# Optimization experiments

Measured on AMD Instinct MI355X. Metric: run time of the kernel, lower is better.

Reference implementation:

```python
import jax, jax.numpy as jnp
import numpy as np

B, N, F, DM, DMO, OM, L = 32, 64, 64, 128, 64, 128, 4
PRE_H, PRE_O, POST_H = 128, 64, 64
E = N * N
EPS = 1e-5


def swish(x):
    return x * jax.nn.sigmoid(x)


def bn_edges(x, g, b):
    # BatchNorm1d(num_features=E) applied to [B, E, D]: per-edge-channel stats over (batch, D)
    m = x.mean(axis=(0, 2), keepdims=True)
    v = x.var(axis=(0, 2), keepdims=True)
    return (x - m) / jnp.sqrt(v + EPS) * g[None, :, None] + b[None, :, None]


def setup_inputs():
    key = jax.random.key(0)
    ks = iter(jax.random.split(key, 64))

    def rn(shape, s=0.05):
        return jax.random.normal(next(ks), shape, dtype=jnp.float32) * s

    # fully-connected graph incl. self-loops (required by BatchNorm1d(n_nodes^2))
    src, dst = np.meshgrid(np.arange(N), np.arange(N), indexing='ij')
    edge_index = jnp.asarray(np.stack([src.reshape(-1), dst.reshape(-1)]), dtype=jnp.int32)
    return {
        'node_feature': rn((B, N, F), 1.0),
        'vectors': rn((B, N, OM), 1.0),
        'edge_index': edge_index,
        'msg_W1': rn((L, 2 * F, DM)), 'msg_b1': rn((L, DM)),
        'bn1_g': jnp.ones((L, E), jnp.float32), 'bn1_b': jnp.zeros((L, E), jnp.float32),
        'msg_W2': rn((L, DM, DM)), 'msg_b2': rn((L, DM)),
        'bn2_g': jnp.ones((L, E), jnp.float32), 'bn2_b': jnp.zeros((L, E), jnp.float32),
        'msg_W3': rn((L, DM, DM)), 'msg_b3': rn((L, DM)),
        'bn3_g': jnp.ones((L, E), jnp.float32), 'bn3_b': jnp.zeros((L, E), jnp.float32),
        'msg_W4': rn((L, DM, DMO)), 'msg_b4': rn((L, DMO)),
        'upd_W1': rn((L, OM + F + DMO, DM)), 'upd_b1': rn((L, DM)),
        'upd_W2': rn((L, DM, DM)), 'upd_b2': rn((L, DM)),
        'upd_W3': rn((L, DM, DM)), 'upd_b3': rn((L, DM)),
        'upd_W4': rn((L, DM, F)), 'upd_b4': rn((L, F)),
        'pre_W1': rn((F, PRE_H)), 'pre_b1': rn((PRE_H,)),
        'pre_W2': rn((PRE_H, PRE_H)), 'pre_b2': rn((PRE_H,)),
        'pre_W3': rn((PRE_H, PRE_H)), 'pre_b3': rn((PRE_H,)),
        'pre_W4': rn((PRE_H, PRE_O)), 'pre_b4': rn((PRE_O,)),
        'post_W1': rn((PRE_O, POST_H)), 'post_b1': rn((POST_H,)),
        'post_W2': rn((POST_H, 1)), 'post_b2': rn((1,)),
    }


def reference(node_feature, vectors, edge_index,
              msg_W1, msg_b1, bn1_g, bn1_b, msg_W2, msg_b2, bn2_g, bn2_b,
              msg_W3, msg_b3, bn3_g, bn3_b, msg_W4, msg_b4,
              upd_W1, upd_b1, upd_W2, upd_b2, upd_W3, upd_b3, upd_W4, upd_b4,
              pre_W1, pre_b1, pre_W2, pre_b2, pre_W3, pre_b3, pre_W4, pre_b4,
              post_W1, post_b1, post_W2, post_b2):
    src, dst = edge_index[0], edge_index[1]
    x = node_feature  # [B, N, F]
    v = vectors       # [B, N, OM]
    cnt = jax.ops.segment_sum(jnp.ones((E,), jnp.float32), dst, num_segments=N)
    inv_cnt = 1.0 / jnp.maximum(cnt, 1.0)
    for l in range(L):
        x_i = x[:, dst]  # [B, E, F] gather targets
        x_j = x[:, src]  # [B, E, F] gather sources
        h = swish(jnp.concatenate([x_i, x_j], -1) @ msg_W1[l] + msg_b1[l])
        h = bn_edges(h, bn1_g[l], bn1_b[l])
        h = bn_edges(swish(h @ msg_W2[l] + msg_b2[l]), bn2_g[l], bn2_b[l])
        h = bn_edges(swish(h @ msg_W3[l] + msg_b3[l]), bn3_g[l], bn3_b[l])
        m = swish(h @ msg_W4[l] + msg_b4[l])  # [B, E, DMO]
        agg = jax.ops.segment_sum(jnp.transpose(m, (1, 0, 2)), dst, num_segments=N)
        agg = jnp.transpose(agg, (1, 0, 2)) * inv_cnt[None, :, None]  # mean aggr, [B, N, DMO]
        u = jnp.concatenate([v, x, agg], -1)  # [B, N, OM+F+DMO]
        h = swish(u @ upd_W1[l] + upd_b1[l])
        h = swish(h @ upd_W2[l] + upd_b2[l])
        h = swish(h @ upd_W3[l] + upd_b3[l])
        x = x + swish(h @ upd_W4[l] + upd_b4[l])  # residual update
    h = swish(x @ pre_W1 + pre_b1)
    h = swish(h @ pre_W2 + pre_b2)
    h = swish(h @ pre_W3 + pre_b3)
    h = h @ pre_W4 + pre_b4
    c = swish(h @ post_W1 + post_b1) @ post_W2 + post_b2  # [B, N, 1]
    x3 = jnp.einsum('bnd,bn->bd', v, c[..., 0])           # coefficient-weighted vector sum
    return x3, v, c
```

## Files before the change

kernel.cpp:

```cpp
#include <hip/hip_runtime.h>
#include <hip/hip_bf16.h>

typedef unsigned short u16t;
typedef __attribute__((ext_vector_type(8))) short bf16x8;
typedef __attribute__((ext_vector_type(4))) float f32x4;

#define Bn 32
#define Nn 64
#define Fd 64
#define DMd 128
#define DMOd 64
#define OMd 128
#define En 4096

#define NTEN 36
#define TOTALC 1073217
#define HP 136
#define UP 264
#define XP 72
#define WSEG 131072

__device__ const int kOffs[NTEN + 1] = {
    0,        131072,   393216,   458752,   459264,   475648,   492032,   557568,
    558080,   574464,   590848,   656384,   656896,   673280,   689664,   722432,
    722688,   853760,   854272,   919808,   920320,   985856,   986368,   1019136,
    1019392,  1027584,  1027712,  1044096,  1044224,  1060608,  1060736,  1068928,
    1068992,  1073088,  1073152,  1073216,  1073217
};

#define C_NF    0
#define C_VEC   131072
#define C_MW1   393216
#define C_MB1   458752
#define C_G1    459264
#define C_BB1   475648
#define C_MW2   492032
#define C_MB2   557568
#define C_G2    558080
#define C_BB2   574464
#define C_MW3   590848
#define C_MB3   656384
#define C_G3    656896
#define C_BB3   673280
#define C_MW4   689664
#define C_MB4   722432
#define C_UW1   722688
#define C_UB1   853760
#define C_UW2   854272
#define C_UB2   919808
#define C_UW3   920320
#define C_UB3   985856
#define C_UW4   986368
#define C_UB4   1019136
#define C_PW1   1019392
#define C_PB1   1027584
#define C_PW2   1027712
#define C_PB2   1044096
#define C_PW3   1044224
#define C_PB3   1060608
#define C_PW4   1060736
#define C_PB4   1068928
#define C_QW1   1068992
#define C_QB1   1073088
#define C_QW2   1073152
#define C_QB2   1073216

#define S_W2T 0
#define S_W3T 16384
#define S_W4T 32768
#define S_U1T 40960
#define S_U2T 73728
#define S_U3T 90112
#define S_U4T 106496
#define S_W1T 114688

struct Ptrs { const void* p[NTEN]; };

__device__ __forceinline__ float us2f(u16t u) {
    return __uint_as_float(((unsigned int)u) << 16);
}
__device__ __forceinline__ u16t f2us(float f) {
    __hip_bfloat16 h = __float2bfloat16(f);
    return *reinterpret_cast<u16t*>(&h);
}
__device__ __forceinline__ u16t f2us_fast(float f) {
    return (u16t)((__float_as_uint(f) + 0x8000u) >> 16);
}
__device__ __forceinline__ unsigned pack2(float f0, float f1) {
    return __builtin_amdgcn_perm(__float_as_uint(f1) + 0x8000u,
                                 __float_as_uint(f0) + 0x8000u, 0x07060302u);
}
__device__ __forceinline__ float swishf(float x) {
    return x * __builtin_amdgcn_rcpf(1.0f + __expf(-x));
}

__global__ void k_flag(const u16t* __restrict__ g1raw, int* __restrict__ flag) {
    if (threadIdx.x == 0) *flag = (g1raw[0] == 0x3F80u) ? 1 : 0;
}

__global__ __launch_bounds__(256) void k_convert(Ptrs t, float* __restrict__ C,
                                                 float* __restrict__ x,
                                                 const int* __restrict__ flagp) {
    int i = blockIdx.x * 256 + threadIdx.x;
    if (i >= TOTALC) return;
    const int flag = *flagp;
    int lo = 0, hi = NTEN;
    while (hi - lo > 1) { int m = (lo + hi) >> 1; if (i >= kOffs[m]) lo = m; else hi = m; }
    const int local = i - kOffs[lo];
    float v;
    if (flag) v = us2f(((const u16t*)t.p[lo])[local]);
    else      v = ((const float*)t.p[lo])[local];
    C[i] = v;
    if (i < Bn * Nn * Fd) x[i] = v;
}

__global__ __launch_bounds__(256) void k_prepw(const float* __restrict__ C,
                                               u16t* __restrict__ W) {
    int i = blockIdx.x * 256 + threadIdx.x;
    if (i >= 4 * WSEG) return;
    const int l = i / WSEG;
    int r = i - l * WSEG;
    int src;
    if (r < S_W3T)      { int q = r;          int n = q >> 7, k = q & 127; src = C_MW2 + l*16384 + k*128 + n; }
    else if (r < S_W4T) { int q = r - S_W3T;  int n = q >> 7, k = q & 127; src = C_MW3 + l*16384 + k*128 + n; }
    else if (r < S_U1T) { int q = r - S_W4T;  int n = q >> 7, k = q & 127; src = C_MW4 + l*8192  + k*64  + n; }
    else if (r < S_U2T) { int q = r - S_U1T;  int n = q >> 8, k = q & 255; src = C_UW1 + l*32768 + k*128 + n; }
    else if (r < S_U3T) { int q = r - S_U2T;  int n = q >> 7, k = q & 127; src = C_UW2 + l*16384 + k*128 + n; }
    else if (r < S_U4T) { int q = r - S_U3T;  int n = q >> 7, k = q & 127; src = C_UW3 + l*16384 + k*128 + n; }
    else if (r < S_W1T) { int q = r - S_U4T;  int n = q >> 7, k = q & 127; src = C_UW4 + l*8192  + k*64  + n; }
    else                { int q = r - S_W1T;  int n = q >> 7, k = q & 127; src = C_MW1 + l*16384 + k*128 + n; }
    W[i] = f2us(C[src]);
}

__global__ __launch_bounds__(128) void k_pq0(const float* __restrict__ x,
                                             const float* __restrict__ W1,
                                             float* __restrict__ P, float* __restrict__ Q) {
    __shared__ float xr[Fd];
    const int bn = blockIdx.x;
    const int tid = threadIdx.x;
    if (tid < Fd) xr[tid] = x[bn * Fd + tid];
    __syncthreads();
    float accP = 0.f, accQ = 0.f;
    #pragma unroll
    for (int k = 0; k < Fd; k++) {
        float xv = xr[k];
        accP += xv * W1[k * DMd + tid];
        accQ += xv * W1[(Fd + k) * DMd + tid];
    }
    P[bn * DMd + tid] = accP;
    Q[bn * DMd + tid] = accQ;
}

__device__ __forceinline__ void red8(float* s, float (*red)[8], float (*stats)[2],
                                     int wv, int lane, int tid) {
    #pragma unroll
    for (int off = 32; off > 0; off >>= 1)
        #pragma unroll
        for (int k = 0; k < 8; k++) s[k] += __shfl_down(s[k], off);
    if (lane == 0) {
        #pragma unroll
        for (int k = 0; k < 8; k++) red[wv][k] = s[k];
    }
    __syncthreads();
    if (tid < 4) {
        float S  = red[0][2*tid]   + red[1][2*tid]   + red[2][2*tid]   + red[3][2*tid];
        float S2 = red[0][2*tid+1] + red[1][2*tid+1] + red[2][2*tid+1] + red[3][2*tid+1];
        float mean = S * (1.0f / 4096.0f);
        float var  = S2 * (1.0f / 4096.0f) - mean * mean;
        stats[tid][0] = mean;
        stats[tid][1] = rsqrtf(var + 1e-5f);
    }
    __syncthreads();
}

__global__ __launch_bounds__(256, 3) void k_edge(
    const float* __restrict__ P, const float* __restrict__ Q,
    const float* __restrict__ b1v,
    const float* __restrict__ g1, const float* __restrict__ bb1,
    const u16t* __restrict__ W2t, const float* __restrict__ b2v,
    const float* __restrict__ g2, const float* __restrict__ bb2,
    const u16t* __restrict__ W3t, const float* __restrict__ b3v,
    const float* __restrict__ g3, const float* __restrict__ bb3,
    const u16t* __restrict__ W4t, const float* __restrict__ b4v,
    float* __restrict__ m_part) {
    __shared__ u16t hE[4][Bn * HP];
    __shared__ float red[4][8];
    __shared__ float stats[4][2];

    const int dst = blockIdx.x & 63, sg = blockIdx.x >> 6, src0 = sg * 4;
    const int tid = threadIdx.x;
    const int wv = tid >> 6, lane = tid & 63, quad = lane >> 4, l15 = lane & 15;
    const int mw = wv & 1, nb2 = wv >> 1;
    const int mrow = mw * 16 + l15;
    const int nBase = nb2 * 64;

    {
        const int b = tid >> 3, d0 = (tid & 7) * 16;
        float4 pv[4], bv[4];
        {
            const float4* pp = (const float4*)&P[(b * Nn + dst) * DMd + d0];
            const float4* bp = (const float4*)&b1v[d0];
            #pragma unroll
            for (int j = 0; j < 4; j++) { pv[j] = pp[j]; bv[j] = bp[j]; }
        }
        float h[4][16];
        #pragma unroll
        for (int e = 0; e < 4; e++) {
            const float4* qq = (const float4*)&Q[(b * Nn + src0 + e) * DMd + d0];
            #pragma unroll
            for (int j = 0; j < 4; j++) {
                float4 qv = qq[j];
                h[e][j*4+0] = swishf(pv[j].x + qv.x + bv[j].x);
                h[e][j*4+1] = swishf(pv[j].y + qv.y + bv[j].y);
                h[e][j*4+2] = swishf(pv[j].z + qv.z + bv[j].z);
                h[e][j*4+3] = swishf(pv[j].w + qv.w + bv[j].w);
            }
        }
        float s[8];
        #pragma unroll
        for (int e = 0; e < 4; e++) {
            float se = 0.f, s2e = 0.f;
            #pragma unroll
            for (int i = 0; i < 16; i++) { se += h[e][i]; s2e += h[e][i] * h[e][i]; }
            s[2*e] = se; s[2*e+1] = s2e;
        }
        red8(s, red, stats, wv, lane, tid);
        #pragma unroll
        for (int e = 0; e < 4; e++) {
            float a  = stats[e][1] * g1[(src0 + e) * Nn + dst];
            float cc = bb1[(src0 + e) * Nn + dst] - stats[e][0] * a;
            uint4 w0, w1;
            w0.x = pack2(h[e][0]  * a + cc, h[e][1]  * a + cc);
            w0.y = pack2(h[e][2]  * a + cc, h[e][3]  * a + cc);
            w0.z = pack2(h[e][4]  * a + cc, h[e][5]  * a + cc);
            w0.w = pack2(h[e][6]  * a + cc, h[e][7]  * a + cc);
            w1.x = pack2(h[e][8]  * a + cc, h[e][9]  * a + cc);
            w1.y = pack2(h[e][10] * a + cc, h[e][11] * a + cc);
            w1.z = pack2(h[e][12] * a + cc, h[e][13] * a + cc);
            w1.w = pack2(h[e][14] * a + cc, h[e][15] * a + cc);
            *(uint4*)&hE[e][b * HP + d0]     = w0;
            *(uint4*)&hE[e][b * HP + d0 + 8] = w1;
        }
    }
    __syncthreads();

    #pragma unroll 1
    for (int st = 0; st < 2; st++) {
        const u16t*  Wt = st ? W3t : W2t;
        const float* bv = st ? b3v : b2v;
        const float* gv = st ? g3  : g2;
        const float* bb = st ? bb3 : bb2;
        f32x4 acc[4][4];
        #pragma unroll
        for (int t = 0; t < 4; t++) {
            float b0 = bv[nBase + t * 16 + l15];
            #pragma unroll
            for (int e = 0; e < 4; e++) acc[e][t] = (f32x4){b0, b0, b0, b0};
        }
        #pragma unroll
        for (int ks = 0; ks < 4; ks++) {
            bf16x8 wb[4];
            #pragma unroll
            for (int t = 0; t < 4; t++)
                wb[t] = *(const bf16x8*)&Wt[(nBase + t * 16 + l15) * 128 + ks * 32 + quad * 8];
            #pragma unroll
            for (int e = 0; e < 4; e++) {
                bf16x8 a8 = *(const bf16x8*)&hE[e][mrow * HP + ks * 32 + quad * 8];
                #pragma unroll
                for (int t = 0; t < 4; t++)
                    acc[e][t] = __builtin_amdgcn_mfma_f32_16x16x32_bf16(a8, wb[t], acc[e][t], 0, 0, 0);
            }
        }
        float s[8];
        #pragma unroll
        for (int e = 0; e < 4; e++) {
            float se = 0.f, s2e = 0.f;
            #pragma unroll
            for (int t = 0; t < 4; t++)
                #pragma unroll
                for (int r = 0; r < 4; r++) {
                    float v = swishf(acc[e][t][r]);
                    acc[e][t][r] = v;
                    se += v; s2e += v * v;
                }
            s[2*e] = se; s[2*e+1] = s2e;
        }
        red8(s, red, stats, wv, lane, tid);
        #pragma unroll
        for (int e = 0; e < 4; e++) {
            float a  = stats[e][1] * gv[(src0 + e) * Nn + dst];
            float cc = bb[(src0 + e) * Nn + dst] - stats[e][0] * a;
            #pragma unroll
            for (int t = 0; t < 4; t++)
                #pragma unroll
                for (int r = 0; r < 4; r++)
                    hE[e][(mw * 16 + quad * 4 + r) * HP + nBase + t * 16 + l15] =
                        f2us_fast(acc[e][t][r] * a + cc);
        }
        __syncthreads();
    }

    {
        const int n40 = nb2 * 32;
        f32x4 a4[4][2];
        #pragma unroll
        for (int t = 0; t < 2; t++) {
            float b0 = b4v[n40 + t * 16 + l15];
            #pragma unroll
            for (int e = 0; e < 4; e++) a4[e][t] = (f32x4){b0, b0, b0, b0};
        }
        #pragma unroll
        for (int ks = 0; ks < 4; ks++) {
            bf16x8 wb[2];
            #pragma unroll
            for (int t = 0; t < 2; t++)
                wb[t] = *(const bf16x8*)&W4t[(n40 + t * 16 + l15) * 128 + ks * 32 + quad * 8];
            #pragma unroll
            for (int e = 0; e < 4; e++) {
                bf16x8 a8 = *(const bf16x8*)&hE[e][mrow * HP + ks * 32 + quad * 8];
                #pragma unroll
                for (int t = 0; t < 2; t++)
                    a4[e][t] = __builtin_amdgcn_mfma_f32_16x16x32_bf16(a8, wb[t], a4[e][t], 0, 0, 0);
            }
        }
        #pragma unroll
        for (int t = 0; t < 2; t++)
            #pragma unroll
            for (int r = 0; r < 4; r++) {
                float m = swishf(a4[0][t][r]) + swishf(a4[1][t][r])
                        + swishf(a4[2][t][r]) + swishf(a4[3][t][r]);
                int b = mw * 16 + quad * 4 + r;
                m_part[(size_t)sg * (Bn * Nn * DMOd) + b * (Nn * DMOd) + dst * DMOd
                       + n40 + t * 16 + l15] = m;
            }
    }
}

__global__ __launch_bounds__(256) void k_updq(
    const float* __restrict__ vC, float* __restrict__ x, const float* __restrict__ m_part,
    const u16t* __restrict__ U1t, const float* __restrict__ b1,
    const u16t* __restrict__ U2t, const float* __restrict__ b2,
    const u16t* __restrict__ U3t, const float* __restrict__ b3,
    const u16t* __restrict__ U4t, const float* __restrict__ b4,
    const u16t* __restrict__ W1Tn, float* __restrict__ Pn, float* __restrict__ Qn,
    int doPQ) {
    __shared__ u16t uL[16 * UP];
    __shared__ u16t hL[16 * HP];
    __shared__ u16t xL[16 * XP];
    __shared__ float aggL[16 * 64];
    const int bl = blockIdx.x;
    const int g0 = bl * 16;
    const int tid = threadIdx.x;
    const int wv = tid >> 6, lane = tid & 63, quad = lane >> 4, l15 = lane & 15;
    const int nBase = wv * 32;

    {
        const int bb = bl >> 2, j0 = (bl & 3) * 16;
        const int o = tid * 4;
        const float* base = m_part + (size_t)bb * (Nn * DMOd) + (j0 + (o >> 6)) * DMOd + (o & 63);
        float4 s = *(const float4*)base;
        #pragma unroll
        for (int sgi = 1; sgi < 16; sgi++) {
            float4 v = *(const float4*)(base + (size_t)sgi * (Bn * Nn * DMOd));
            s.x += v.x; s.y += v.y; s.z += v.z; s.w += v.w;
        }
        *(float4*)&aggL[o] = s;
    }
    __syncthreads();

    {
        const int i = tid >> 4, c0 = (tid & 15) * 16;
        const int g = g0 + i;
        const float* srcp; float scl = 1.f;
        if (c0 < 128)       srcp = &vC[g * OMd + c0];
        else if (c0 < 192)  srcp = &x[g * Fd + (c0 - 128)];
        else              { srcp = &aggL[i * 64 + (c0 - 192)]; scl = 1.0f / 64.0f; }
        uint4 s0, s1;
        s0.x = pack2(srcp[0]  * scl, srcp[1]  * scl);
        s0.y = pack2(srcp[2]  * scl, srcp[3]  * scl);
        s0.z = pack2(srcp[4]  * scl, srcp[5]  * scl);
        s0.w = pack2(srcp[6]  * scl, srcp[7]  * scl);
        s1.x = pack2(srcp[8]  * scl, srcp[9]  * scl);
        s1.y = pack2(srcp[10] * scl, srcp[11] * scl);
        s1.z = pack2(srcp[12] * scl, srcp[13] * scl);
        s1.w = pack2(srcp[14] * scl, srcp[15] * scl);
        *(uint4*)&uL[i * UP + c0]     = s0;
        *(uint4*)&uL[i * UP + c0 + 8] = s1;
    }
    __syncthreads();

    {
        f32x4 acc[2];
        #pragma unroll
        for (int t = 0; t < 2; t++) {
            float b0 = b1[nBase + t * 16 + l15];
            acc[t] = (f32x4){b0, b0, b0, b0};
        }
        #pragma unroll
        for (int ks = 0; ks < 8; ks++) {
            bf16x8 a8 = *(const bf16x8*)&uL[l15 * UP + ks * 32 + quad * 8];
            #pragma unroll
            for (int t = 0; t < 2; t++) {
                bf16x8 b8 = *(const bf16x8*)&U1t[(nBase + t * 16 + l15) * 256 + ks * 32 + quad * 8];
                acc[t] = __builtin_amdgcn_mfma_f32_16x16x32_bf16(a8, b8, acc[t], 0, 0, 0);
            }
        }
        #pragma unroll
        for (int t = 0; t < 2; t++)
            #pragma unroll
            for (int r = 0; r < 4; r++)
                hL[(quad * 4 + r) * HP + nBase + t * 16 + l15] = f2us_fast(swishf(acc[t][r]));
    }
    __syncthreads();

    #pragma unroll 1
    for (int st = 0; st < 2; st++) {
        const u16t*  Ut = st ? U3t : U2t;
        const float* bb = st ? b3  : b2;
        f32x4 acc[2];
        #pragma unroll
        for (int t = 0; t < 2; t++) {
            float b0 = bb[nBase + t * 16 + l15];
            acc[t] = (f32x4){b0, b0, b0, b0};
        }
        #pragma unroll
        for (int ks = 0; ks < 4; ks++) {
            bf16x8 a8 = *(const bf16x8*)&hL[l15 * HP + ks * 32 + quad * 8];
            #pragma unroll
            for (int t = 0; t < 2; t++) {
                bf16x8 b8 = *(const bf16x8*)&Ut[(nBase + t * 16 + l15) * 128 + ks * 32 + quad * 8];
                acc[t] = __builtin_amdgcn_mfma_f32_16x16x32_bf16(a8, b8, acc[t], 0, 0, 0);
            }
        }
        __syncthreads();
        #pragma unroll
        for (int t = 0; t < 2; t++)
            #pragma unroll
            for (int r = 0; r < 4; r++)
                hL[(quad * 4 + r) * HP + nBase + t * 16 + l15] = f2us_fast(swishf(acc[t][r]));
        __syncthreads();
    }

    {
        const int n4 = wv * 16;
        f32x4 acc;
        {
            float b0 = b4[n4 + l15];
            acc = (f32x4){b0, b0, b0, b0};
        }
        #pragma unroll
        for (int ks = 0; ks < 4; ks++) {
            bf16x8 a8 = *(const bf16x8*)&hL[l15 * HP + ks * 32 + quad * 8];
            bf16x8 b8 = *(const bf16x8*)&U4t[(n4 + l15) * 128 + ks * 32 + quad * 8];
            acc = __builtin_amdgcn_mfma_f32_16x16x32_bf16(a8, b8, acc, 0, 0, 0);
        }
        #pragma unroll
        for (int r = 0; r < 4; r++) {
            int row = quad * 4 + r, col = n4 + l15;
            float xn = x[(g0 + row) * Fd + col] + swishf(acc[r]);
            x[(g0 + row) * Fd + col] = xn;
            xL[row * XP + col] = f2us_fast(xn);
        }
    }
    __syncthreads();

    if (doPQ) {
        f32x4 ap[2], aq[2];
        #pragma unroll
        for (int j = 0; j < 2; j++) { ap[j] = (f32x4){0,0,0,0}; aq[j] = (f32x4){0,0,0,0}; }
        #pragma unroll
        for (int ks = 0; ks < 2; ks++) {
            bf16x8 a8 = *(const bf16x8*)&xL[l15 * XP + ks * 32 + quad * 8];
            #pragma unroll
            for (int j = 0; j < 2; j++) {
                const int n0 = (wv * 2 + j) * 16 + l15;
                bf16x8 bp = *(const bf16x8*)&W1Tn[n0 * 128 + ks * 32 + quad * 8];
                bf16x8 bq = *(const bf16x8*)&W1Tn[n0 * 128 + 64 + ks * 32 + quad * 8];
                ap[j] = __builtin_amdgcn_mfma_f32_16x16x32_bf16(a8, bp, ap[j], 0, 0, 0);
                aq[j] = __builtin_amdgcn_mfma_f32_16x16x32_bf16(a8, bq, aq[j], 0, 0, 0);
            }
        }
        #pragma unroll
        for (int j = 0; j < 2; j++)
            #pragma unroll
            for (int r = 0; r < 4; r++) {
                int g = g0 + quad * 4 + r, col = (wv * 2 + j) * 16 + l15;
                Pn[g * DMd + col] = ap[j][r];
                Qn[g * DMd + col] = aq[j][r];
            }
    }
}

__global__ __launch_bounds__(128) void k_final(
    const float* __restrict__ x, const void* __restrict__ vraw,
    const float* __restrict__ pW1, const float* __restrict__ pb1,
    const float* __restrict__ pW2, const float* __restrict__ pb2,
    const float* __restrict__ pW3, const float* __restrict__ pb3,
    const float* __restrict__ pW4, const float* __restrict__ pb4,
    const float* __restrict__ qW1, const float* __restrict__ qb1,
    const float* __restrict__ qW2, const float* __restrict__ qb2,
    float* __restrict__ c_buf, void* __restrict__ out, const int* __restrict__ flagp) {
    __shared__ float xr[64];
    __shared__ float ha[128];
    __shared__ float hb[128];
    __shared__ float hc[64];
    __shared__ float tt[64];
    const int bn = blockIdx.x;
    const int tid = threadIdx.x;
    const int flag = *flagp;
    if (tid < 64) xr[tid] = x[bn * Fd + tid];
    __syncthreads();
    float acc = pb1[tid];
    #pragma unroll 8
    for (int k = 0; k < 64; k++) acc += xr[k] * pW1[k * 128 + tid];
    ha[tid] = swishf(acc);
    __syncthreads();
    acc = pb2[tid];
    #pragma unroll 8
    for (int k = 0; k < 128; k++) acc += ha[k] * pW2[k * 128 + tid];
    hb[tid] = swishf(acc);
    __syncthreads();
    acc = pb3[tid];
    #pragma unroll 8
    for (int k = 0; k < 128; k++) acc += hb[k] * pW3[k * 128 + tid];
    ha[tid] = swishf(acc);
    __syncthreads();
    if (tid < 64) {
        acc = pb4[tid];
        #pragma unroll 8
        for (int k = 0; k < 128; k++) acc += ha[k] * pW4[k * 64 + tid];
        hc[tid] = acc;
    }
    __syncthreads();
    if (tid < 64) {
        acc = qb1[tid];
        #pragma unroll 8
        for (int k = 0; k < 64; k++) acc += hc[k] * qW1[k * 64 + tid];
        tt[tid] = swishf(acc);
    }
    __syncthreads();
    if (tid < 64) {
        float p = tt[tid] * qW2[tid];
        #pragma unroll
        for (int off = 32; off > 0; off >>= 1) p += __shfl_down(p, off);
        if (tid == 0) {
            float cv = p + qb2[0];
            c_buf[bn] = cv;
            const int ci = 4096 + Bn * Nn * OMd + bn;
            if (flag) ((u16t*)out)[ci] = f2us(cv);
            else      ((float*)out)[ci] = cv;
        }
    }
    const int vi = bn * OMd + tid;
    if (flag) ((u16t*)out)[4096 + vi] = ((const u16t*)vraw)[vi];
    else      ((float*)out)[4096 + vi] = ((const float*)vraw)[vi];
}

__global__ __launch_bounds__(128) void k_x3(const float* __restrict__ vC,
                                            const float* __restrict__ c_buf,
                                            void* __restrict__ out,
                                            const int* __restrict__ flagp) {
    const int b = blockIdx.x, d = threadIdx.x;
    const int flag = *flagp;
    float acc = 0.f;
    #pragma unroll 4
    for (int n = 0; n < Nn; n++)
        acc += vC[(b * Nn + n) * OMd + d] * c_buf[b * Nn + n];
    if (flag) ((u16t*)out)[b * OMd + d] = f2us(acc);
    else      ((float*)out)[b * OMd + d] = acc;
}

extern "C" void kernel_launch(void* const* d_in, const int* in_sizes, int n_in,
                              void* d_out, int out_size, void* d_ws, size_t ws_size,
                              hipStream_t stream) {
    float* ws = (float*)d_ws;
    int*   flag   = (int*)d_ws;
    float* C      = ws + 16;
    float* x      = C + 1073664;
    float* P      = x + 131072;
    float* Q      = P + 262144;
    float* m_part = Q + 262144;
    float* c_buf  = m_part + 2097152;
    u16t*  Wt     = (u16t*)(c_buf + 2048);

    Ptrs t;
    for (int i = 0, j = 0; i < 37; i++) {
        if (i == 2) continue;
        t.p[j++] = d_in[i];
    }

    k_flag<<<1, 64, 0, stream>>>((const u16t*)d_in[5], flag);
    k_convert<<<(TOTALC + 255) / 256, 256, 0, stream>>>(t, C, x, flag);
    k_prepw<<<(4 * WSEG + 255) / 256, 256, 0, stream>>>(C, Wt);
    k_pq0<<<Bn * Nn, 128, 0, stream>>>(x, C + C_MW1, P, Q);

    for (int l = 0; l < 4; l++) {
        u16t* Wl = Wt + l * WSEG;
        k_edge<<<64 * 16, 256, 0, stream>>>(
            P, Q,
            C + C_MB1 + l * DMd, C + C_G1 + l * En, C + C_BB1 + l * En,
            Wl + S_W2T, C + C_MB2 + l * DMd, C + C_G2 + l * En, C + C_BB2 + l * En,
            Wl + S_W3T, C + C_MB3 + l * DMd, C + C_G3 + l * En, C + C_BB3 + l * En,
            Wl + S_W4T, C + C_MB4 + l * DMOd,
            m_part);
        const int doPQ = (l < 3) ? 1 : 0;
        const u16t* W1Tn = Wt + (doPQ ? (l + 1) : 0) * WSEG + S_W1T;
        k_updq<<<Bn * Nn / 16, 256, 0, stream>>>(
            C + C_VEC, x, m_part,
            Wl + S_U1T, C + C_UB1 + l * DMd,
            Wl + S_U2T, C + C_UB2 + l * DMd,
            Wl + S_U3T, C + C_UB3 + l * DMd,
            Wl + S_U4T, C + C_UB4 + l * DMOd,
            W1Tn, P, Q, doPQ);
    }

    k_final<<<Bn * Nn, 128, 0, stream>>>(x, d_in[1],
        C + C_PW1, C + C_PB1, C + C_PW2, C + C_PB2,
        C + C_PW3, C + C_PB3, C + C_PW4, C + C_PB4,
        C + C_QW1, C + C_QB1, C + C_QW2, C + C_QB2,
        c_buf, d_out, flag);
    k_x3<<<Bn, 128, 0, stream>>>(C + C_VEC, c_buf, d_out, flag);
}
```

Baseline: 392.3 us.

## Fold batchnorm affine into following GEMM epilogue and split aggregation kernel

The edge kernel now stores the un-normalized swish activations to shared memory and applies each batchnorm's per-edge scale and shift after the next matmul. It uses precomputed weight column sums (a new k_colsum kernel) so that shift*colsum + bias is added in the epilogue. This removes one barrier per stage, because the stats reduction now overlaps the shared-memory writes. The 16-way partial-sum reduction of m_part moves out of the update kernel into a separate k_agg kernel, which adds a launch and a global round trip per layer. Normalizing after the bf16 rounding changes numerics slightly.

```diff
diff --git a/kernel.cpp b/kernel.cpp
--- a/kernel.cpp
+++ b/kernel.cpp
@@ -132,6 +132,29 @@
     W[i] = f2us(C[src]);
 }
 
+__global__ __launch_bounds__(256) void k_colsum(const float* __restrict__ C,
+                                                float* __restrict__ csum) {
+    int i = blockIdx.x * 256 + threadIdx.x;
+    if (i >= 4 * 320) return;
+    const int l = i / 320;
+    int r = i - l * 320;
+    float s = 0.f;
+    if (r < 128) {
+        const float* w = C + C_MW2 + l * 16384 + r;
+        #pragma unroll 8
+        for (int k = 0; k < 128; k++) s += w[k * 128];
+    } else if (r < 256) {
+        const float* w = C + C_MW3 + l * 16384 + (r - 128);
+        #pragma unroll 8
+        for (int k = 0; k < 128; k++) s += w[k * 128];
+    } else {
+        const float* w = C + C_MW4 + l * 8192 + (r - 256);
+        #pragma unroll 8
+        for (int k = 0; k < 128; k++) s += w[k * 64];
+    }
+    csum[i] = s;
+}
+
 __global__ __launch_bounds__(128) void k_pq0(const float* __restrict__ x,
                                              const float* __restrict__ W1,
                                              float* __restrict__ P, float* __restrict__ Q) {
@@ -151,8 +174,7 @@
     Q[bn * DMd + tid] = accQ;
 }
 
-__device__ __forceinline__ void red8(float* s, float (*red)[8], float (*stats)[2],
-                                     int wv, int lane, int tid) {
+__device__ __forceinline__ void redpart1(float* s, float (*red)[8], int wv, int lane) {
     #pragma unroll
     for (int off = 32; off > 0; off >>= 1)
         #pragma unroll
@@ -162,15 +184,17 @@
         for (int k = 0; k < 8; k++) red[wv][k] = s[k];
     }
     __syncthreads();
-    if (tid < 4) {
-        float S  = red[0][2*tid]   + red[1][2*tid]   + red[2][2*tid]   + red[3][2*tid];
-        float S2 = red[0][2*tid+1] + red[1][2*tid+1] + red[2][2*tid+1] + red[3][2*tid+1];
-        float mean = S * (1.0f / 4096.0f);
-        float var  = S2 * (1.0f / 4096.0f) - mean * mean;
-        stats[tid][0] = mean;
-        stats[tid][1] = rsqrtf(var + 1e-5f);
-    }
-    __syncthreads();
+}
+__device__ __forceinline__ void stats_all(const float (*red)[8], float* mean, float* istd) {
+    #pragma unroll
+    for (int e = 0; e < 4; e++) {
+        float S  = red[0][2*e]   + red[1][2*e]   + red[2][2*e]   + red[3][2*e];
+        float S2 = red[0][2*e+1] + red[1][2*e+1] + red[2][2*e+1] + red[3][2*e+1];
+        float m = S * (1.0f / 4096.0f);
+        float v = S2 * (1.0f / 4096.0f) - m * m;
+        mean[e] = m;
+        istd[e] = rsqrtf(v + 1e-5f);
+    }
 }
 
 __global__ __launch_bounds__(256, 3) void k_edge(
@@ -182,10 +206,10 @@
     const u16t* __restrict__ W3t, const float* __restrict__ b3v,
     const float* __restrict__ g3, const float* __restrict__ bb3,
     const u16t* __restrict__ W4t, const float* __restrict__ b4v,
+    const float* __restrict__ cs,
     float* __restrict__ m_part) {
     __shared__ u16t hE[4][Bn * HP];
     __shared__ float red[4][8];
-    __shared__ float stats[4][2];
 
     const int dst = blockIdx.x & 63, sg = blockIdx.x >> 6, src0 = sg * 4;
     const int tid = threadIdx.x;
@@ -194,6 +218,8 @@
     const int mrow = mw * 16 + l15;
     const int nBase = nb2 * 64;
 
+    float mean[4], istd[4];
+
     {
         const int b = tid >> 3, d0 = (tid & 7) * 16;
         float4 pv[4], bv[4];
@@ -203,60 +229,55 @@
             #pragma unroll
             for (int j = 0; j < 4; j++) { pv[j] = pp[j]; bv[j] = bp[j]; }
         }
-        float h[4][16];
+        float s[8];
+        #pragma unroll
+        for (int k = 0; k < 8; k++) s[k] = 0.f;
         #pragma unroll
         for (int e = 0; e < 4; e++) {
             const float4* qq = (const float4*)&Q[(b * Nn + src0 + e) * DMd + d0];
+            float h[16];
             #pragma unroll
             for (int j = 0; j < 4; j++) {
                 float4 qv = qq[j];
-                h[e][j*4+0] = swishf(pv[j].x + qv.x + bv[j].x);
-                h[e][j*4+1] = swishf(pv[j].y + qv.y + bv[j].y);
-                h[e][j*4+2] = swishf(pv[j].z + qv.z + bv[j].z);
-                h[e][j*4+3] = swishf(pv[j].w + qv.w + bv[j].w);
-            }
-        }
-        float s[8];
-        #pragma unroll
-        for (int e = 0; e < 4; e++) {
+                h[j*4+0] = swishf(pv[j].x + qv.x + bv[j].x);
+                h[j*4+1] = swishf(pv[j].y + qv.y + bv[j].y);
+                h[j*4+2] = swishf(pv[j].z + qv.z + bv[j].z);
+                h[j*4+3] = swishf(pv[j].w + qv.w + bv[j].w);
+            }
             float se = 0.f, s2e = 0.f;
             #pragma unroll
-            for (int i = 0; i < 16; i++) { se += h[e][i]; s2e += h[e][i] * h[e][i]; }
+            for (int i = 0; i < 16; i++) { se += h[i]; s2e += h[i] * h[i]; }
             s[2*e] = se; s[2*e+1] = s2e;
-        }
-        red8(s, red, stats, wv, lane, tid);
-        #pragma unroll
-        for (int e = 0; e < 4; e++) {
-            float a  = stats[e][1] * g1[(src0 + e) * Nn + dst];
-            float cc = bb1[(src0 + e) * Nn + dst] - stats[e][0] * a;
             uint4 w0, w1;
-            w0.x = pack2(h[e][0]  * a + cc, h[e][1]  * a + cc);
-            w0.y = pack2(h[e][2]  * a + cc, h[e][3]  * a + cc);
-            w0.z = pack2(h[e][4]  * a + cc, h[e][5]  * a + cc);
-            w0.w = pack2(h[e][6]  * a + cc, h[e][7]  * a + cc);
-            w1.x = pack2(h[e][8]  * a + cc, h[e][9]  * a + cc);
-            w1.y = pack2(h[e][10] * a + cc, h[e][11] * a + cc);
-            w1.z = pack2(h[e][12] * a + cc, h[e][13] * a + cc);
-            w1.w = pack2(h[e][14] * a + cc, h[e][15] * a + cc);
+            w0.x = pack2(h[0],  h[1]);  w0.y = pack2(h[2],  h[3]);
+            w0.z = pack2(h[4],  h[5]);  w0.w = pack2(h[6],  h[7]);
+            w1.x = pack2(h[8],  h[9]);  w1.y = pack2(h[10], h[11]);
+            w1.z = pack2(h[12], h[13]); w1.w = pack2(h[14], h[15]);
             *(uint4*)&hE[e][b * HP + d0]     = w0;
             *(uint4*)&hE[e][b * HP + d0 + 8] = w1;
         }
-    }
-    __syncthreads();
+        redpart1(s, red, wv, lane);
+        stats_all(red, mean, istd);
+    }
 
     #pragma unroll 1
     for (int st = 0; st < 2; st++) {
-        const u16t*  Wt = st ? W3t : W2t;
-        const float* bv = st ? b3v : b2v;
-        const float* gv = st ? g3  : g2;
-        const float* bb = st ? bb3 : bb2;
+        const u16t*  Wt  = st ? W3t : W2t;
+        const float* bnv = st ? b3v : b2v;
+        const float* csn = st ? (cs + 128) : cs;
+        const float* gP  = st ? g2  : g1;
+        const float* bbP = st ? bb2 : bb1;
+        float aP[4], cP[4];
+        #pragma unroll
+        for (int e = 0; e < 4; e++) {
+            aP[e] = istd[e] * gP[(src0 + e) * Nn + dst];
+            cP[e] = bbP[(src0 + e) * Nn + dst] - mean[e] * aP[e];
+        }
         f32x4 acc[4][4];
         #pragma unroll
-        for (int t = 0; t < 4; t++) {
-            float b0 = bv[nBase + t * 16 + l15];
-            #pragma unroll
-            for (int e = 0; e < 4; e++) acc[e][t] = (f32x4){b0, b0, b0, b0};
-        }
+        for (int e = 0; e < 4; e++)
+            #pragma unroll
+            for (int t = 0; t < 4; t++) acc[e][t] = (f32x4){0.f, 0.f, 0.f, 0.f};
         #pragma unroll
         for (int ks = 0; ks < 4; ks++) {
             bf16x8 wb[4];
@@ -271,7 +292,17 @@
                     acc[e][t] = __builtin_amdgcn_mfma_f32_16x16x32_bf16(a8, wb[t], acc[e][t], 0, 0, 0);
             }
         }
+        float k2[4][4];
+        #pragma unroll
+        for (int t = 0; t < 4; t++) {
+            int col = nBase + t * 16 + l15;
+            float csv = csn[col], bv0 = bnv[col];
+            #pragma unroll
+            for (int e = 0; e < 4; e++) k2[e][t] = fmaf(cP[e], csv, bv0);
+        }
         float s[8];
+        #pragma unroll
+        for (int k = 0; k < 8; k++) s[k] = 0.f;
         #pragma unroll
         for (int e = 0; e < 4; e++) {
             float se = 0.f, s2e = 0.f;
@@ -279,36 +310,38 @@
             for (int t = 0; t < 4; t++)
                 #pragma unroll
                 for (int r = 0; r < 4; r++) {
-                    float v = swishf(acc[e][t][r]);
+                    float v = swishf(fmaf(aP[e], acc[e][t][r], k2[e][t]));
                     acc[e][t][r] = v;
                     se += v; s2e += v * v;
                 }
             s[2*e] = se; s[2*e+1] = s2e;
         }
-        red8(s, red, stats, wv, lane, tid);
-        #pragma unroll
-        for (int e = 0; e < 4; e++) {
-            float a  = stats[e][1] * gv[(src0 + e) * Nn + dst];
-            float cc = bb[(src0 + e) * Nn + dst] - stats[e][0] * a;
+        __syncthreads();
+        #pragma unroll
+        for (int e = 0; e < 4; e++)
             #pragma unroll
             for (int t = 0; t < 4; t++)
                 #pragma unroll
                 for (int r = 0; r < 4; r++)
                     hE[e][(mw * 16 + quad * 4 + r) * HP + nBase + t * 16 + l15] =
-                        f2us_fast(acc[e][t][r] * a + cc);
-        }
-        __syncthreads();
+                        f2us_fast(acc[e][t][r]);
+        redpart1(s, red, wv, lane);
+        stats_all(red, mean, istd);
     }
 
     {
         const int n40 = nb2 * 32;
+        float aP[4], cP[4];
+        #pragma unroll
+        for (int e = 0; e < 4; e++) {
+            aP[e] = istd[e] * g3[(src0 + e) * Nn + dst];
+            cP[e] = bb3[(src0 + e) * Nn + dst] - mean[e] * aP[e];
+        }
         f32x4 a4[4][2];
         #pragma unroll
-        for (int t = 0; t < 2; t++) {
-            float b0 = b4v[n40 + t * 16 + l15];
-            #pragma unroll
-            for (int e = 0; e < 4; e++) a4[e][t] = (f32x4){b0, b0, b0, b0};
-        }
+        for (int e = 0; e < 4; e++)
+            #pragma unroll
+            for (int t = 0; t < 2; t++) a4[e][t] = (f32x4){0.f, 0.f, 0.f, 0.f};
         #pragma unroll
         for (int ks = 0; ks < 4; ks++) {
             bf16x8 wb[2];
@@ -324,20 +357,34 @@
             }
         }
         #pragma unroll
-        for (int t = 0; t < 2; t++)
+        for (int t = 0; t < 2; t++) {
+            int col = n40 + t * 16 + l15;
+            float csv = cs[256 + col], bv0 = b4v[col];
             #pragma unroll
             for (int r = 0; r < 4; r++) {
-                float m = swishf(a4[0][t][r]) + swishf(a4[1][t][r])
-                        + swishf(a4[2][t][r]) + swishf(a4[3][t][r]);
+                float m = 0.f;
+                #pragma unroll
+                for (int e = 0; e < 4; e++)
+                    m += swishf(fmaf(aP[e], a4[e][t][r], fmaf(cP[e], csv, bv0)));
                 int b = mw * 16 + quad * 4 + r;
-                m_part[(size_t)sg * (Bn * Nn * DMOd) + b * (Nn * DMOd) + dst * DMOd
-                       + n40 + t * 16 + l15] = m;
-            }
-    }
+                m_part[(size_t)sg * (Bn * Nn * DMOd) + b * (Nn * DMOd) + dst * DMOd + col] = m;
+            }
+        }
+    }
+}
+
+__global__ __launch_bounds__(256) void k_agg(const float* __restrict__ m_part,
+                                             float* __restrict__ agg) {
+    const int o = blockIdx.x * 256 + threadIdx.x;
+    float s = 0.f;
+    #pragma unroll
+    for (int sg = 0; sg < 16; sg++)
+        s += m_part[(size_t)sg * (Bn * Nn * DMOd) + o];
+    agg[o] = s;
 }
 
 __global__ __launch_bounds__(256) void k_updq(
-    const float* __restrict__ vC, float* __restrict__ x, const float* __restrict__ m_part,
+    const float* __restrict__ vC, float* __restrict__ x, const float* __restrict__ agg,
     const u16t* __restrict__ U1t, const float* __restrict__ b1,
     const u16t* __restrict__ U2t, const float* __restrict__ b2,
     const u16t* __restrict__ U3t, const float* __restrict__ b3,
@@ -347,26 +394,10 @@
     __shared__ u16t uL[16 * UP];
     __shared__ u16t hL[16 * HP];
     __shared__ u16t xL[16 * XP];
-    __shared__ float aggL[16 * 64];
-    const int bl = blockIdx.x;
-    const int g0 = bl * 16;
+    const int g0 = blockIdx.x * 16;
     const int tid = threadIdx.x;
     const int wv = tid >> 6, lane = tid & 63, quad = lane >> 4, l15 = lane & 15;
     const int nBase = wv * 32;
-
-    {
-        const int bb = bl >> 2, j0 = (bl & 3) * 16;
-        const int o = tid * 4;
-        const float* base = m_part + (size_t)bb * (Nn * DMOd) + (j0 + (o >> 6)) * DMOd + (o & 63);
-        float4 s = *(const float4*)base;
-        #pragma unroll
-        for (int sgi = 1; sgi < 16; sgi++) {
-            float4 v = *(const float4*)(base + (size_t)sgi * (Bn * Nn * DMOd));
-            s.x += v.x; s.y += v.y; s.z += v.z; s.w += v.w;
-        }
-        *(float4*)&aggL[o] = s;
-    }
-    __syncthreads();
 
     {
         const int i = tid >> 4, c0 = (tid & 15) * 16;
@@ -374,7 +405,7 @@
         const float* srcp; float scl = 1.f;
         if (c0 < 128)       srcp = &vC[g * OMd + c0];
         else if (c0 < 192)  srcp = &x[g * Fd + (c0 - 128)];
-        else              { srcp = &aggL[i * 64 + (c0 - 192)]; scl = 1.0f / 64.0f; }
+        else              { srcp = &agg[g * DMOd + (c0 - 192)]; scl = 1.0f / 64.0f; }
         uint4 s0, s1;
         s0.x = pack2(srcp[0]  * scl, srcp[1]  * scl);
         s0.y = pack2(srcp[2]  * scl, srcp[3]  * scl);
@@ -580,8 +611,10 @@
     float* P      = x + 131072;
     float* Q      = P + 262144;
     float* m_part = Q + 262144;
-    float* c_buf  = m_part + 2097152;
-    u16t*  Wt     = (u16t*)(c_buf + 2048);
+    float* agg    = m_part + 2097152;
+    float* c_buf  = agg + 131072;
+    float* csum   = c_buf + 2048;
+    u16t*  Wt     = (u16t*)(csum + 2048);
 
     Ptrs t;
     for (int i = 0, j = 0; i < 37; i++) {
@@ -592,6 +625,7 @@
     k_flag<<<1, 64, 0, stream>>>((const u16t*)d_in[5], flag);
     k_convert<<<(TOTALC + 255) / 256, 256, 0, stream>>>(t, C, x, flag);
     k_prepw<<<(4 * WSEG + 255) / 256, 256, 0, stream>>>(C, Wt);
+    k_colsum<<<5, 256, 0, stream>>>(C, csum);
     k_pq0<<<Bn * Nn, 128, 0, stream>>>(x, C + C_MW1, P, Q);
 
     for (int l = 0; l < 4; l++) {
@@ -602,11 +636,13 @@
             Wl + S_W2T, C + C_MB2 + l * DMd, C + C_G2 + l * En, C + C_BB2 + l * En,
             Wl + S_W3T, C + C_MB3 + l * DMd, C + C_G3 + l * En, C + C_BB3 + l * En,
             Wl + S_W4T, C + C_MB4 + l * DMOd,
+            csum + l * 320,
             m_part);
+        k_agg<<<512, 256, 0, stream>>>(m_part, agg);
         const int doPQ = (l < 3) ? 1 : 0;
         const u16t* W1Tn = Wt + (doPQ ? (l + 1) : 0) * WSEG + S_W1T;
         k_updq<<<Bn * Nn / 16, 256, 0, stream>>>(
-            C + C_VEC, x, m_part,
+            C + C_VEC, x, agg,
             Wl + S_U1T, C + C_UB1 + l * DMd,
             Wl + S_U2T, C + C_UB2 + l * DMd,
             Wl + S_U3T, C + C_UB3 + l * DMd,
```

New measurement: 398.9 us. About the same (+1.7%).
